# Kernel optimization log

Hardware: AMD Instinct MI355X
Metric: run time of the kernel (lower is better)

## Reference

```python
import jax, jax.numpy as jnp
import numpy as np

B, L, K = 16, 8192, 128


def setup_inputs() -> dict:
    key = jax.random.key(0)
    k1, k2, k3 = jax.random.split(key, 3)
    # tracer positions in [-pi, pi]
    x0 = (jax.random.uniform(k1, (B, L), dtype=jnp.float32) * 2.0 - 1.0) * jnp.pi
    y0 = (jax.random.uniform(k2, (B, L), dtype=jnp.float32) * 2.0 - 1.0) * jnp.pi
    psi = jax.random.normal(k3, (B, K, K), dtype=jnp.float32)
    return {"x0": x0, "y0": y0, "psi": psi}


def reference(x0, y0, psi):
    # x0, y0: (B, L) float32; psi: (B, K, K) float32
    Kdim = psi.shape[-1]
    # wavenumbers, fftshifted, matching torch.fft.fftshift(torch.fft.fftfreq(K, d=1/K))
    kx = jnp.fft.fftshift(jnp.fft.fftfreq(Kdim, d=1.0 / Kdim)).astype(jnp.float32)
    ky = kx  # identical construction
    # fftshifted 2D spectrum: psi_hat[b, i, j] pairs with phase x*kx[j] + y*ky[i]
    # (torch meshgrid indexing='xy': KX[i,j]=kx[j], KY[i,j]=ky[i])
    psi_hat = jnp.fft.fftshift(jnp.fft.fft2(psi), axes=(-2, -1)).astype(jnp.complex64)
    # separable phase: exp(i(x*kx_j + y*ky_i)) = Ex[b,l,j] * Ey[b,l,i]
    Ex = jnp.exp(1j * (x0[..., None] * kx)).astype(jnp.complex64)  # (B, L, K)
    Ey = jnp.exp(1j * (y0[..., None] * ky)).astype(jnp.complex64)  # (B, L, K)
    # contract j first: (B, L, K) intermediate instead of (B, L, K*K)
    tmp = jnp.einsum('bij,blj->bli', psi_hat, Ex)
    psi_x = jnp.real(jnp.einsum('bli,bli->bl', tmp, Ey)) / (Kdim ** 2)
    return psi_x.astype(jnp.float32)
```

## Files before the change

kernel.cpp:

```cpp
#include <hip/hip_runtime.h>
#include <math.h>

#ifndef M_PI
#define M_PI 3.14159265358979323846
#endif

typedef _Float16 half8v __attribute__((ext_vector_type(8)));
typedef _Float16 half2v __attribute__((ext_vector_type(2)));
typedef float float4v __attribute__((ext_vector_type(4)));

constexpr int KDIM = 128;
constexpr int LTOT = 8192;
constexpr int TILE_L = 64;
constexpr int NT = 256;
constexpr int WSTR = 136;

__global__ __launch_bounds__(256) void cb_kernel(const float* __restrict__ psi,
                                                 float* __restrict__ cb) {
    __shared__ float red[4];
    const int b = blockIdx.x >> 4;
    const int slice = blockIdx.x & 15;
    const float* P = psi + (size_t)b * 16384 + slice * 1024;
    const int t = threadIdx.x;
    float4v v = *(const float4v*)(P + t * 4);
    float s = (v.x - v.y) + (v.z - v.w);
    const int e = slice * 1024 + t * 4;
    if ((e >> 7) & 1) s = -s;
    for (int off = 1; off < 64; off <<= 1) s += __shfl_xor(s, off, 64);
    if ((t & 63) == 0) red[t >> 6] = s;
    __syncthreads();
    if (t == 0) atomicAdd(&cb[b], (red[0] + red[1]) + (red[2] + red[3]));
}

__global__ __launch_bounds__(NT, 3) void main_kernel(const float* __restrict__ x0,
        const float* __restrict__ y0, const float* __restrict__ psi,
        const float* __restrict__ cbv, float* __restrict__ out) {
    __shared__ _Float16 wxT[TILE_L][WSTR];
    __shared__ _Float16 wyT[TILE_L][WSTR];
    __shared__ float cbq[KDIM], sbq[KDIM];
    __shared__ float ndh[KDIM], ndl[KDIM], ndh2[KDIM], ndl2[KDIM];
    __shared__ float posA[2][TILE_L], s64A[2][TILE_L], saA[2][TILE_L], caA[2][TILE_L];
    __shared__ float partial[4][TILE_L];

    const int tid = threadIdx.x;
    const int lane = tid & 63;
    const int w = tid >> 6;
    const int bid = blockIdx.x;
    const int b = bid >> 7;
    const int l0 = (bid & 127) * TILE_L;
    const int qd = lane >> 4;
    const int ln = lane & 15;

    const float* Pb = psi + (size_t)b * 16384;

    float4v a_raw[2][2];
#pragma unroll
    for (int mi = 0; mi < 2; ++mi) {
        const float* rp = Pb + (32 * w + 16 * mi + ln) * 128 + 8 * qd;
        a_raw[mi][0] = *(const float4v*)(rp);
        a_raw[mi][1] = *(const float4v*)(rp + 4);
    }

    if (tid < KDIM) {
        float bq = (float)tid * (float)(M_PI / 128.0);
        float sn, cs;
        sincosf(bq, &sn, &cs);
        sbq[tid] = sn; cbq[tid] = cs;
        double d = (double)tid * (M_PI / 64.0);
        float h = (float)d, l = (float)(d - (double)h);
        ndh[tid] = h; ndl[tid] = l;
        double d2 = d - 2.0 * M_PI;
        float h2 = (float)d2, l2 = (float)(d2 - (double)h2);
        ndh2[tid] = h2; ndl2[tid] = l2;
    } else {
        const int m = tid - KDIM;
        const int ax = m >> 6;
        const int l = m & 63;
        const float* src = ax ? y0 : x0;
        float pos = src[(size_t)b * LTOT + l0 + l];
        posA[ax][l] = pos;
        s64A[ax][l] = sinf(64.0f * pos);
        float sa, ca;
        sincosf(0.5f * pos, &sa, &ca);
        saA[ax][l] = sa; caA[ax][l] = ca;
    }
    __syncthreads();

    const float step = (float)(M_PI / 64.0);
    for (int it = 0; it < 32; ++it) {
        const int i = tid + NT * it;
        const int mat = i >> 12;
        const int r = i & 4095;
        const int l = r >> 6;
        const int qp = r & 63;
        const int q0 = qp << 1;
        const float pos = posA[mat][l];
        const float s64 = s64A[mat][l];
        const float sa = saA[mat][l], ca = caA[mat][l];
        _Float16 wpair[2];
#pragma unroll
        for (int j = 0; j < 2; ++j) {
            const int q = q0 + j;
            const float cq = cbq[q], sq = sbq[q];
            float sn = sa * cq - ca * sq;
            float cs = ca * cq + sa * sq;
            float num = (q & 1) ? -s64 : s64;
            float wv;
            if (__builtin_expect(fabsf(sn) >= 1e-3f, 1)) {
                wv = num * cs * __builtin_amdgcn_rcpf(sn);
            } else {
                float ta = pos - step * (float)q;
                float nh, nl;
                if (ta > -1.0f) { nh = ndh[q];  nl = ndl[q]; }
                else            { nh = ndh2[q]; nl = ndl2[q]; }
                float u = (pos - nh) - nl;
                if (fabsf(u) < 1e-7f) {
                    wv = 128.0f;
                } else {
                    float hh = 0.5f * u;
                    float s2 = hh * (1.0f - 0.16666667f * hh * hh);
                    float c2 = 1.0f - 0.5f * hh * hh;
                    wv = num * c2 * __builtin_amdgcn_rcpf(s2);
                }
            }
            wpair[j] = (_Float16)wv;
        }
        _Float16* dst = mat ? &wyT[0][0] : &wxT[0][0];
        *(half2v*)&dst[l * WSTR + q0] = *(half2v*)wpair;
    }
    __syncthreads();

    float4v acc[2][4];
#pragma unroll
    for (int mi = 0; mi < 2; ++mi)
#pragma unroll
        for (int ni = 0; ni < 4; ++ni) acc[mi][ni] = (float4v){0.f, 0.f, 0.f, 0.f};

#pragma unroll
    for (int k = 0; k < 4; ++k) {
        half8v af[2];
#pragma unroll
        for (int mi = 0; mi < 2; ++mi) {
#pragma unroll
            for (int j = 0; j < 4; ++j) {
                af[mi][j]     = (_Float16)a_raw[mi][0][j];
                af[mi][4 + j] = (_Float16)a_raw[mi][1][j];
            }
        }
        if (k < 3) {
#pragma unroll
            for (int mi = 0; mi < 2; ++mi) {
                const float* rp = Pb + (32 * w + 16 * mi + ln) * 128 + (k + 1) * 32 + 8 * qd;
                a_raw[mi][0] = *(const float4v*)(rp);
                a_raw[mi][1] = *(const float4v*)(rp + 4);
            }
        }
#pragma unroll
        for (int ni = 0; ni < 4; ++ni) {
            half8v bf = *(const half8v*)&wxT[16 * ni + ln][k * 32 + 8 * qd];
#pragma unroll
            for (int mi = 0; mi < 2; ++mi)
                acc[mi][ni] = __builtin_amdgcn_mfma_f32_16x16x32_f16(af[mi], bf, acc[mi][ni], 0, 0, 0);
        }
    }

    float part[4];
#pragma unroll
    for (int ni = 0; ni < 4; ++ni) {
        float s = 0.f;
#pragma unroll
        for (int mi = 0; mi < 2; ++mi) {
            const _Float16* wp = &wyT[16 * ni + ln][32 * w + 16 * mi + 4 * qd];
            half2v w01 = *(const half2v*)(wp);
            half2v w23 = *(const half2v*)(wp + 2);
            s += acc[mi][ni][0] * (float)w01[0] + acc[mi][ni][1] * (float)w01[1]
               + acc[mi][ni][2] * (float)w23[0] + acc[mi][ni][3] * (float)w23[1];
        }
        s += __shfl_xor(s, 16, 64);
        s += __shfl_xor(s, 32, 64);
        part[ni] = s;
    }
    if (qd == 0) {
#pragma unroll
        for (int ni = 0; ni < 4; ++ni) partial[w][16 * ni + ln] = part[ni];
    }
    __syncthreads();

    if (tid < TILE_L) {
        float s = (partial[0][tid] + partial[1][tid]) + (partial[2][tid] + partial[3][tid]);
        s -= s64A[0][tid] * s64A[1][tid] * cbv[b];
        out[(size_t)b * LTOT + l0 + tid] = s * (1.0f / 16384.0f);
    }
}

extern "C" void kernel_launch(void* const* d_in, const int* in_sizes, int n_in,
                              void* d_out, int out_size, void* d_ws, size_t ws_size,
                              hipStream_t stream) {
    const float* x0  = (const float*)d_in[0];
    const float* y0  = (const float*)d_in[1];
    const float* psi = (const float*)d_in[2];
    float* out = (float*)d_out;
    float* cb  = (float*)d_ws;

    hipMemsetAsync(d_ws, 0, 16 * sizeof(float), stream);
    cb_kernel<<<256, 256, 0, stream>>>(psi, cb);
    main_kernel<<<16 * (LTOT / TILE_L), NT, 0, stream>>>(x0, y0, psi, cb, out);
}
```

Baseline: 92.00 us.

## Generate weight tables by angle-addition recurrence per thread instead of table lookups

Each thread now owns one position row and 64 wavenumbers, computing sin/cos of the shifted half-angle by a rotation recurrence (step pi/128, re-seeded every 16 with a pi/8 rotation) instead of reading precomputed cos/sin tables from shared memory per element. Weights are written as 8-wide half vectors rather than half2 pairs, and the per-position shared arrays plus one table setup phase are removed. This is meant to cut LDS traffic and index arithmetic in the weight generation phase. The recurrence accumulates rounding error, which is why the small-denominator fallback threshold was raised, and there is a risk of accuracy drift near singular points. The psi prefetch is now issued after the weight build, so its latency is less hidden.

```diff
diff --git a/kernel.cpp b/kernel.cpp
--- a/kernel.cpp
+++ b/kernel.cpp
@@ -37,9 +37,8 @@
         const float* __restrict__ cbv, float* __restrict__ out) {
     __shared__ _Float16 wxT[TILE_L][WSTR];
     __shared__ _Float16 wyT[TILE_L][WSTR];
-    __shared__ float cbq[KDIM], sbq[KDIM];
     __shared__ float ndh[KDIM], ndl[KDIM], ndh2[KDIM], ndl2[KDIM];
-    __shared__ float posA[2][TILE_L], s64A[2][TILE_L], saA[2][TILE_L], caA[2][TILE_L];
+    __shared__ float s64A[2][TILE_L];
     __shared__ float partial[4][TILE_L];
 
     const int tid = threadIdx.x;
@@ -53,6 +52,75 @@
 
     const float* Pb = psi + (size_t)b * 16384;
 
+    if (tid < KDIM) {
+        double d = (double)tid * (M_PI / 64.0);
+        float h = (float)d;
+        ndh[tid] = h; ndl[tid] = (float)(d - (double)h);
+        double d2 = d - 2.0 * M_PI;
+        float h2 = (float)d2;
+        ndh2[tid] = h2; ndl2[tid] = (float)(d2 - (double)h2);
+    }
+
+    const int col = tid & 127;
+    const int mat = col >> 6;
+    const int l = col & 63;
+    const int hf = tid >> 7;
+    const float* src = mat ? y0 : x0;
+    const float pos = src[(size_t)b * LTOT + l0 + l];
+    const float s64 = sinf(64.0f * pos);
+    float sa, ca;
+    sincosf(0.5f * pos, &sa, &ca);
+    float cs_s, cs_c;
+    if (hf == 0) { cs_s = sa; cs_c = ca; s64A[mat][l] = s64; }
+    else         { cs_s = -ca; cs_c = sa; }
+    __syncthreads();
+
+    _Float16* dst = mat ? &wyT[l][0] : &wxT[l][0];
+    const float CB  = 0.9996988186962042f,  SB  = 0.024541228522912288f;
+    const float C16 = 0.9238795325112867f,  S16 = 0.3826834323650898f;
+    const float step = (float)(M_PI / 64.0);
+#pragma unroll
+    for (int kk = 0; kk < 4; ++kk) {
+        float ws_ = cs_s, wc_ = cs_c;
+        const int q0 = 64 * hf + 16 * kk;
+#pragma unroll
+        for (int h8 = 0; h8 < 2; ++h8) {
+            _Float16 buf[8];
+#pragma unroll
+            for (int j = 0; j < 8; ++j) {
+                const int q = q0 + 8 * h8 + j;
+                const float num = (j & 1) ? -s64 : s64;
+                float wv;
+                if (__builtin_expect(fabsf(ws_) >= 2e-3f, 1)) {
+                    wv = num * wc_ * __builtin_amdgcn_rcpf(ws_);
+                } else {
+                    float ta = pos - step * (float)q;
+                    float nh, nl;
+                    if (ta > -1.0f) { nh = ndh[q];  nl = ndl[q]; }
+                    else            { nh = ndh2[q]; nl = ndl2[q]; }
+                    float u = (pos - nh) - nl;
+                    if (fabsf(u) < 1e-7f) {
+                        wv = 128.0f;
+                    } else {
+                        float hh = 0.5f * u;
+                        float s2 = hh * (1.0f - 0.16666667f * hh * hh);
+                        float c2 = 1.0f - 0.5f * hh * hh;
+                        wv = num * c2 * __builtin_amdgcn_rcpf(s2);
+                    }
+                }
+                buf[j] = (_Float16)wv;
+                float ns = ws_ * CB - wc_ * SB;
+                wc_ = wc_ * CB + ws_ * SB;
+                ws_ = ns;
+            }
+            *(half8v*)&dst[q0 + 8 * h8] = *(half8v*)buf;
+        }
+        float ns = cs_s * C16 - cs_c * S16;
+        cs_c = cs_c * C16 + cs_s * S16;
+        cs_s = ns;
+    }
+    __syncthreads();
+
     float4v a_raw[2][2];
 #pragma unroll
     for (int mi = 0; mi < 2; ++mi) {
@@ -60,75 +128,6 @@
         a_raw[mi][0] = *(const float4v*)(rp);
         a_raw[mi][1] = *(const float4v*)(rp + 4);
     }
-
-    if (tid < KDIM) {
-        float bq = (float)tid * (float)(M_PI / 128.0);
-        float sn, cs;
-        sincosf(bq, &sn, &cs);
-        sbq[tid] = sn; cbq[tid] = cs;
-        double d = (double)tid * (M_PI / 64.0);
-        float h = (float)d, l = (float)(d - (double)h);
-        ndh[tid] = h; ndl[tid] = l;
-        double d2 = d - 2.0 * M_PI;
-        float h2 = (float)d2, l2 = (float)(d2 - (double)h2);
-        ndh2[tid] = h2; ndl2[tid] = l2;
-    } else {
-        const int m = tid - KDIM;
-        const int ax = m >> 6;
-        const int l = m & 63;
-        const float* src = ax ? y0 : x0;
-        float pos = src[(size_t)b * LTOT + l0 + l];
-        posA[ax][l] = pos;
-        s64A[ax][l] = sinf(64.0f * pos);
-        float sa, ca;
-        sincosf(0.5f * pos, &sa, &ca);
-        saA[ax][l] = sa; caA[ax][l] = ca;
-    }
-    __syncthreads();
-
-    const float step = (float)(M_PI / 64.0);
-    for (int it = 0; it < 32; ++it) {
-        const int i = tid + NT * it;
-        const int mat = i >> 12;
-        const int r = i & 4095;
-        const int l = r >> 6;
-        const int qp = r & 63;
-        const int q0 = qp << 1;
-        const float pos = posA[mat][l];
-        const float s64 = s64A[mat][l];
-        const float sa = saA[mat][l], ca = caA[mat][l];
-        _Float16 wpair[2];
-#pragma unroll
-        for (int j = 0; j < 2; ++j) {
-            const int q = q0 + j;
-            const float cq = cbq[q], sq = sbq[q];
-            float sn = sa * cq - ca * sq;
-            float cs = ca * cq + sa * sq;
-            float num = (q & 1) ? -s64 : s64;
-            float wv;
-            if (__builtin_expect(fabsf(sn) >= 1e-3f, 1)) {
-                wv = num * cs * __builtin_amdgcn_rcpf(sn);
-            } else {
-                float ta = pos - step * (float)q;
-                float nh, nl;
-                if (ta > -1.0f) { nh = ndh[q];  nl = ndl[q]; }
-                else            { nh = ndh2[q]; nl = ndl2[q]; }
-                float u = (pos - nh) - nl;
-                if (fabsf(u) < 1e-7f) {
-                    wv = 128.0f;
-                } else {
-                    float hh = 0.5f * u;
-                    float s2 = hh * (1.0f - 0.16666667f * hh * hh);
-                    float c2 = 1.0f - 0.5f * hh * hh;
-                    wv = num * c2 * __builtin_amdgcn_rcpf(s2);
-                }
-            }
-            wpair[j] = (_Float16)wv;
-        }
-        _Float16* dst = mat ? &wyT[0][0] : &wxT[0][0];
-        *(half2v*)&dst[l * WSTR + q0] = *(half2v*)wpair;
-    }
-    __syncthreads();
 
     float4v acc[2][4];
 #pragma unroll
```

Measured after the change: 88.52 us. -3.8%, faster.
